# Performance work log

Measured on AMD Instinct MI355X. Metric: run time of the kernel, lower is better.

The kernel has to match this reference:

```python
import jax, jax.numpy as jnp
import numpy as np

B, N, C = 8, 4096, 768
H, M = 12, 64          # num_heads, num_landmarks
D = C // H             # head_dim = 64


def setup_inputs() -> dict:
    key = jax.random.key(0)
    k1, k2, k3, k4 = jax.random.split(key, 4)
    s = 0.02
    return {
        "x": jax.random.normal(k1, (B, N, C), dtype=jnp.float32),
        "w_qkv": jax.random.normal(k2, (3 * C, C), dtype=jnp.float32) * s,
        "w_proj": jax.random.normal(k3, (C, C), dtype=jnp.float32) * s,
        "b_proj": jax.random.normal(k4, (C,), dtype=jnp.float32) * s,
    }


def iterative_inv(mat, n_iter=6):
    # mat: [B, H, M, M]; Newton-Schulz cubic iteration for pseudo-inverse
    I = jnp.eye(mat.shape[-1], dtype=mat.dtype)
    K = mat
    # init: K^T / max_j(sum_i K_ij)  per (B,H)
    scale = jnp.max(jnp.sum(K, axis=-2), axis=-1)[:, :, None, None]
    V = jnp.swapaxes(K, -1, -2) / scale
    for _ in range(n_iter):
        KV = K @ V
        V = 0.25 * V @ (13.0 * I - KV @ (15.0 * I - KV @ (7.0 * I - KV)))
    return V


def reference(x, w_qkv, w_proj, b_proj):
    b, n, c = x.shape
    qkv = (x @ w_qkv.T).reshape(b, n, 3, H, D).transpose(2, 0, 3, 1, 4)  # [3,B,H,N,D]
    Q, K, V = qkv[0], qkv[1], qkv[2]
    Q = Q / (D ** 0.5)
    # landmark pooling (N % M == 0 path): segment means of length N//M
    Kl = K.reshape(b, H, M, n // M, D).mean(axis=-2)  # [B,H,M,D]
    Ql = Q.reshape(b, H, M, n // M, D).mean(axis=-2)  # [B,H,M,D]
    kernel1 = jax.nn.softmax(jnp.einsum('bhnd,bhmd->bhnm', Q, Kl), axis=-1)   # [B,H,N,M]
    kernel2 = jax.nn.softmax(jnp.einsum('bhmd,bhld->bhml', Ql, Kl), axis=-1)  # [B,H,M,M]
    kernel3 = jax.nn.softmax(jnp.einsum('bhmd,bhnd->bhmn', Ql, K), axis=-1)   # [B,H,M,N]
    SV = (kernel1 @ iterative_inv(kernel2)) @ (kernel3 @ V)  # [B,H,N,D]
    SV = SV.transpose(0, 2, 1, 3).reshape(b, n, c)
    out = SV @ w_proj.T + b_proj
    out = out + V.transpose(0, 2, 1, 3).reshape(b, n, c)
    return out
```

## Files before the change

kernel.cpp:

```cpp
#include <hip/hip_runtime.h>
#include <hip/hip_bf16.h>
#include <stdint.h>

typedef __bf16 bf16;
typedef __bf16 bf16x8 __attribute__((ext_vector_type(8)));
typedef __bf16 bf16x4 __attribute__((ext_vector_type(4)));
typedef float f32x4 __attribute__((ext_vector_type(4)));

#define B_ 8
#define N_ 4096
#define C_ 768
#define H_ 12
#define M_ 64
#define D_ 64
#define NT_ 32768
#define C3_ 2304

typedef __attribute__((address_space(3))) void lds_void_t;
typedef const __attribute__((address_space(1))) void gvoid_t;

__device__ __forceinline__ void gl_lds16(const void* gsrc, void* ldst) {
  __builtin_amdgcn_global_load_lds((gvoid_t*)(uintptr_t)gsrc,
                                   (lds_void_t*)(uintptr_t)ldst, 16, 0, 0);
}

__device__ __forceinline__ f32x4 mfma16(bf16x8 a, bf16x8 b, f32x4 c) {
  return __builtin_amdgcn_mfma_f32_16x16x32_bf16(a, b, c, 0, 0, 0);
}

#define VMW8 asm volatile("s_waitcnt vmcnt(8)" ::: "memory")
#define VMW4 asm volatile("s_waitcnt vmcnt(4)" ::: "memory")
#define VMW0 asm volatile("s_waitcnt vmcnt(0)" ::: "memory")
#define RAWBAR() { __builtin_amdgcn_sched_barrier(0); __builtin_amdgcn_s_barrier(); __builtin_amdgcn_sched_barrier(0); }

#define NX4   6291456
#define NW14  442368
#define NW24  147456
__global__ void k_cvt3(const float* __restrict__ x, bf16* __restrict__ xo,
                       const float* __restrict__ w1, bf16* __restrict__ w1o,
                       const float* __restrict__ w2, bf16* __restrict__ w2o) {
  const int stride = gridDim.x * blockDim.x;
  for (int i = blockIdx.x * blockDim.x + threadIdx.x; i < NX4 + NW14 + NW24; i += stride) {
    const float* src; bf16* dst; int idx;
    if (i < NX4)              { src = x;  dst = xo;  idx = i; }
    else if (i < NX4 + NW14)  { src = w1; dst = w1o; idx = i - NX4; }
    else                      { src = w2; dst = w2o; idx = i - NX4 - NW14; }
    f32x4 v = *(const f32x4*)(src + (size_t)idx * 4);
    bf16x4 o;
    o[0] = (bf16)v[0]; o[1] = (bf16)v[1]; o[2] = (bf16)v[2]; o[3] = (bf16)v[3];
    *(bf16x4*)(dst + (size_t)idx * 4) = o;
  }
}

__global__ __launch_bounds__(512, 2) void k_qkv(
    const bf16* __restrict__ xbf, const bf16* __restrict__ wbf,
    bf16* __restrict__ Qb, bf16* __restrict__ Kb, bf16* __restrict__ Vb,
    float* __restrict__ Qlf, float* __restrict__ Klf)
{
  __shared__ bf16 As[4][8192];
  __shared__ bf16 Bs[4][8192];
  const int t = threadIdx.x;
  const int wave = t >> 6, lane = t & 63;
  const int l15 = lane & 15, l16 = lane >> 4;

  const int bid = blockIdx.x;
  const int swz = (bid & 7) * 144 + (bid >> 3);
  const int bt = swz / 9, ct = swz % 9;
  const int row0 = bt * 256, ct0 = ct * 256;
  const int wr = wave >> 2, wc = wave & 3;

  const int srow = t >> 2;
  const int scol = (((t & 3) ^ ((t >> 3) & 3)) << 3);
  const bf16* gaBase = xbf + (size_t)(row0 + srow) * C_ + scol;
  const bf16* gbBase = wbf + (size_t)(ct0 + srow) * C_ + scol;

  const int aoff = (wr * 128 + l15) * 32 + ((l16 ^ ((l15 >> 1) & 3)) << 3);
  const int boff = (wc * 64 + l15) * 32 + ((l16 ^ ((l15 >> 1) & 3)) << 3);

  f32x4 acc[8][4] = {};
  bf16x8 afr0[4], afr1[4], bfr[2][4];

#define QSTAGE(kt3) {                                                            \
    const int sb_ = (kt3) & 3;                                                   \
    gl_lds16(gaBase + (kt3) * 32, &As[sb_][t * 8]);                              \
    gl_lds16(gbBase + (kt3) * 32, &Bs[sb_][t * 8]);                              \
    gl_lds16(gaBase + (size_t)128 * C_ + (kt3) * 32, &As[sb_][(t + 512) * 8]);   \
    gl_lds16(gbBase + (size_t)128 * C_ + (kt3) * 32, &Bs[sb_][(t + 512) * 8]); }

#define QKSTEP(kt, DO_STAGE, DO_NXT, VMW_, DO_BAR) {                             \
    if (DO_STAGE) QSTAGE((kt) + 3);                                             \
    { const bf16* asC = As[(kt) & 3];                                            \
      _Pragma("unroll")                                                          \
      for (int i = 0; i < 4; ++i)                                                \
        afr1[i] = *(const bf16x8*)&asC[aoff + (4 + i) * 512]; }                  \
    __builtin_amdgcn_s_setprio(1);                                               \
    _Pragma("unroll")                                                            \
    for (int i = 0; i < 4; ++i)                                                  \
      _Pragma("unroll")                                                          \
      for (int j = 0; j < 4; ++j)                                                \
        acc[i][j] = mfma16(afr0[i], bfr[(kt) & 1][j], acc[i][j]);                \
    __builtin_amdgcn_s_setprio(0);                                               \
    if (DO_NXT) {                                                                \
      const bf16* asN = As[((kt) + 1) & 3];                                      \
      const bf16* bsN = Bs[((kt) + 1) & 3];                                      \
      _Pragma("unroll")                                                          \
      for (int i = 0; i < 4; ++i)                                                \
        afr0[i] = *(const bf16x8*)&asN[aoff + i * 512];                          \
      _Pragma("unroll")                                                          \
      for (int j = 0; j < 4; ++j)                                                \
        bfr[((kt) + 1) & 1][j] = *(const bf16x8*)&bsN[boff + j * 512]; }         \
    __builtin_amdgcn_s_setprio(1);                                               \
    _Pragma("unroll")                                                            \
    for (int i = 0; i < 4; ++i)                                                  \
      _Pragma("unroll")                                                          \
      for (int j = 0; j < 4; ++j)                                                \
        acc[4 + i][j] = mfma16(afr1[i], bfr[(kt) & 1][j], acc[4 + i][j]);        \
    __builtin_amdgcn_s_setprio(0);                                               \
    VMW_;                                                                        \
    if (DO_BAR) RAWBAR(); }

  QSTAGE(0); QSTAGE(1); QSTAGE(2);
  VMW4;
  RAWBAR();
#pragma unroll
  for (int i = 0; i < 4; ++i) afr0[i] = *(const bf16x8*)&As[0][aoff + i * 512];
#pragma unroll
  for (int j = 0; j < 4; ++j) bfr[0][j] = *(const bf16x8*)&Bs[0][boff + j * 512];

  QKSTEP(0, 1, 1, VMW4, 1)  QKSTEP(1, 1, 1, VMW4, 1)  QKSTEP(2, 1, 1, VMW4, 1)
  QKSTEP(3, 1, 1, VMW4, 1)  QKSTEP(4, 1, 1, VMW4, 1)  QKSTEP(5, 1, 1, VMW4, 1)
  QKSTEP(6, 1, 1, VMW4, 1)  QKSTEP(7, 1, 1, VMW4, 1)  QKSTEP(8, 1, 1, VMW4, 1)
  QKSTEP(9, 1, 1, VMW4, 1)  QKSTEP(10, 1, 1, VMW4, 1) QKSTEP(11, 1, 1, VMW4, 1)
  QKSTEP(12, 1, 1, VMW4, 1) QKSTEP(13, 1, 1, VMW4, 1) QKSTEP(14, 1, 1, VMW4, 1)
  QKSTEP(15, 1, 1, VMW4, 1) QKSTEP(16, 1, 1, VMW4, 1) QKSTEP(17, 1, 1, VMW4, 1)
  QKSTEP(18, 1, 1, VMW4, 1) QKSTEP(19, 1, 1, VMW4, 1) QKSTEP(20, 1, 1, VMW4, 1)
  QKSTEP(21, 0, 1, VMW0, 1)
  QKSTEP(22, 0, 1, (void)0, 1)
  QKSTEP(23, 0, 0, (void)0, 0)

#undef QKSTEP
#undef QSTAGE

  const int colblock = ct0 + wc * 64;
  const int which = colblock / C_;
  const int h = (colblock % C_) / D_;
  const int b = row0 >> 12;
  const int n_base = (row0 & (N_ - 1)) + wr * 128;
  bf16* dst = (which == 0) ? Qb : (which == 1) ? Kb : Vb;
  const float scale = (which == 0) ? 0.125f : 1.0f;
  const size_t base = ((size_t)(b * H_ + h) * N_ + n_base) * D_;
#pragma unroll
  for (int i = 0; i < 8; ++i)
#pragma unroll
    for (int q = 0; q < 4; ++q) {
      const int rloc = i * 16 + l16 * 4 + q;
#pragma unroll
      for (int j = 0; j < 4; ++j) {
        const int d = j * 16 + l15;
        dst[base + (size_t)rloc * D_ + d] = (bf16)(acc[i][j][q] * scale);
      }
    }
  if (which < 2) {
    float* lmout = (which == 0) ? Qlf : Klf;
#pragma unroll
    for (int g = 0; g < 2; ++g) {
      const int m = (n_base >> 6) + g;
#pragma unroll
      for (int j = 0; j < 4; ++j) {
        float s = 0.f;
#pragma unroll
        for (int i = 4 * g; i < 4 * g + 4; ++i)
#pragma unroll
          for (int q = 0; q < 4; ++q) s += acc[i][j][q];
        s *= scale;
        s += __shfl_xor(s, 16);
        s += __shfl_xor(s, 32);
        if (l16 == 0)
          lmout[((size_t)(b * H_ + h) * M_ + m) * D_ + j * 16 + lane] = s * (1.0f / 64.0f);
      }
    }
  }
}

__global__ __launch_bounds__(512, 1) void k_inv(
    const float* __restrict__ Qlf, const float* __restrict__ Klf,
    float* __restrict__ pinv, bf16* __restrict__ Qlb, bf16* __restrict__ Klb)
{
  __shared__ float K2[4096];
  __shared__ float Vm[4096];
  __shared__ float KV[4096];
  __shared__ float T1[4096];
  __shared__ float U1[4096];
  __shared__ float tmp64[64];
  __shared__ float sscale;
  const int t = threadIdx.x;
  const int bh = blockIdx.x;
  const size_t off = (size_t)bh * 4096;
  for (int idx = t; idx < 4096; idx += 512) {
    const float q = Qlf[off + idx];
    T1[idx] = q;
    Qlb[off + idx] = (bf16)q;
  }
  for (int idx = t; idx < 4096; idx += 512) {
    const int r = idx >> 6, c = idx & 63;
    const float k = Klf[off + idx];
    U1[c * 64 + r] = k;
    Klb[off + idx] = (bf16)k;
  }
  __syncthreads();
  const int j0 = (t & 15) * 4;
  const int i0 = (t >> 4) * 2;

  auto MMstep = [&](const float* A, const float* Bm, float* O, float dg, float sg, float al) {
    float r2[2][4] = {};
    for (int k = 0; k < 64; ++k) {
      f32x4 bv = *(const f32x4*)&Bm[k * 64 + j0];
      const float a0 = A[(i0 + 0) * 64 + k];
      const float a1 = A[(i0 + 1) * 64 + k];
#pragma unroll
      for (int jj = 0; jj < 4; ++jj) { r2[0][jj] += a0 * bv[jj]; r2[1][jj] += a1 * bv[jj]; }
    }
#pragma unroll
    for (int ii = 0; ii < 2; ++ii)
#pragma unroll
      for (int jj = 0; jj < 4; ++jj)
        O[(i0 + ii) * 64 + j0 + jj] = al * (dg * A[(i0 + ii) * 64 + (j0 + jj)] + sg * r2[ii][jj]);
    __syncthreads();
  };

  {
    float r2[2][4] = {};
    for (int k = 0; k < 64; ++k) {
      f32x4 bv = *(const f32x4*)&U1[k * 64 + j0];
      const float a0 = T1[(i0 + 0) * 64 + k];
      const float a1 = T1[(i0 + 1) * 64 + k];
#pragma unroll
      for (int jj = 0; jj < 4; ++jj) { r2[0][jj] += a0 * bv[jj]; r2[1][jj] += a1 * bv[jj]; }
    }
#pragma unroll
    for (int ii = 0; ii < 2; ++ii)
#pragma unroll
      for (int jj = 0; jj < 4; ++jj)
        K2[(i0 + ii) * 64 + j0 + jj] = __expf(r2[ii][jj]);
  }
  __syncthreads();
  if (t < 64) {
    float s = 0.f;
    for (int k = 0; k < 64; ++k) s += K2[t * 64 + k];
    tmp64[t] = 1.0f / s;
  }
  __syncthreads();
  for (int idx = t; idx < 4096; idx += 512) K2[idx] *= tmp64[idx >> 6];
  __syncthreads();
  if (t < 64) {
    float s = 0.f;
    for (int i = 0; i < 64; ++i) s += K2[i * 64 + t];
    tmp64[t] = s;
  }
  __syncthreads();
  if (t == 0) {
    float mx = tmp64[0];
    for (int j2 = 1; j2 < 64; ++j2) mx = fmaxf(mx, tmp64[j2]);
    sscale = 1.0f / mx;
  }
  __syncthreads();
  for (int idx = t; idx < 4096; idx += 512) {
    const int r = idx >> 6, c = idx & 63;
    Vm[idx] = K2[c * 64 + r] * sscale;
  }
  __syncthreads();

  float* pV = Vm;
  float* pT = T1;
  for (int it = 0; it < 6; ++it) {
    MMstep(K2, pV, KV, 0.f, 1.f, 1.f);
    MMstep(KV, KV, pT, 7.f, -1.f, 1.f);
    MMstep(KV, pT, U1, 15.f, -1.f, 1.f);
    MMstep(pV, U1, pT, 13.f, -1.f, 0.25f);
    float* sw = pV; pV = pT; pT = sw;
  }
  for (int idx = t; idx < 4096; idx += 512) pinv[off + idx] = pV[idx];
}

__global__ __launch_bounds__(256, 2) void k_k3v(
    const bf16* __restrict__ Qlb, const bf16* __restrict__ Kb, const bf16* __restrict__ Vb,
    float* __restrict__ Zpart, float* __restrict__ rspart)
{
  __shared__ bf16 Qls[64 * 64];
  __shared__ bf16 Ks[128 * 64];
  __shared__ bf16 Vs[128 * 64];
  __shared__ bf16 Ps[64 * 128];
  __shared__ float rs[64];
  const int t = threadIdx.x, wave = t >> 6, lane = t & 63;
  const int l15 = lane & 15, l16 = lane >> 4;
  const int key = l15 & 7;
  const int bh = blockIdx.x >> 3;
  const int chunk = blockIdx.x & 7;
  const size_t kvbase = (size_t)bh * N_ * D_ + (size_t)chunk * 512 * D_;
  const int srow8 = t >> 3;
  const int ssw = (((t & 7) ^ ((t >> 3) & 7)) << 3);
  {
    const bf16* g = Qlb + (size_t)bh * 4096;
    gl_lds16(g + (size_t)srow8 * 64 + ssw, &Qls[t * 8]);
    gl_lds16(g + (size_t)(32 + srow8) * 64 + ssw, &Qls[(t + 256) * 8]);
  }
  if (t < 64) rs[t] = 0.f;
  f32x4 z[4] = {};
  for (int st = 0; st < 4; ++st) {
    const bf16* gk = Kb + kvbase + (size_t)st * 128 * D_;
    const bf16* gv = Vb + kvbase + (size_t)st * 128 * D_;
#pragma unroll
    for (int c = 0; c < 4; ++c) {
      gl_lds16(gk + (size_t)(c * 32 + srow8) * 64 + ssw, &Ks[(t + c * 256) * 8]);
      gl_lds16(gv + (t + c * 256) * 8, &Vs[(t + c * 256) * 8]);
    }
    __syncthreads();
    f32x4 sacc[4][2] = {};
#pragma unroll
    for (int kk = 0; kk < 2; ++kk) {
      bf16x8 af[4], bk[2];
#pragma unroll
      for (int i = 0; i < 4; ++i)
        af[i] = *(const bf16x8*)&Qls[(i * 16 + l15) * 64 + (((kk * 4 + l16) ^ key) << 3)];
#pragma unroll
      for (int j2 = 0; j2 < 2; ++j2)
        bk[j2] = *(const bf16x8*)&Ks[(wave * 32 + j2 * 16 + l15) * 64 + (((kk * 4 + l16) ^ key) << 3)];
#pragma unroll
      for (int i = 0; i < 4; ++i)
#pragma unroll
        for (int j2 = 0; j2 < 2; ++j2)
          sacc[i][j2] = mfma16(af[i], bk[j2], sacc[i][j2]);
    }
#pragma unroll
    for (int i = 0; i < 4; ++i)
#pragma unroll
      for (int q = 0; q < 4; ++q) {
        const float e0 = __expf(sacc[i][0][q]);
        const float e1 = __expf(sacc[i][1][q]);
        const int m = i * 16 + l16 * 4 + q;
        const int mk = m & 7;
        Ps[m * 128 + ((((wave * 4 + (l15 >> 3)) ^ mk) << 3) | (l15 & 7))] = (bf16)e0;
        Ps[m * 128 + ((((wave * 4 + 2 + (l15 >> 3)) ^ mk) << 3) | (l15 & 7))] = (bf16)e1;
        float p = e0 + e1;
        p += __shfl_xor(p, 1); p += __shfl_xor(p, 2);
        p += __shfl_xor(p, 4); p += __shfl_xor(p, 8);
        if (l15 == 0) atomicAdd(&rs[m], p);
      }
    __syncthreads();
#pragma unroll
    for (int kk = 0; kk < 4; ++kk) {
      const int kbase = kk * 32 + 8 * l16;
      const int d = wave * 16 + l15;
      bf16x8 bv;
#pragma unroll
      for (int e = 0; e < 8; ++e) bv[e] = Vs[(kbase + e) * 64 + d];
#pragma unroll
      for (int i = 0; i < 4; ++i) {
        bf16x8 ap = *(const bf16x8*)&Ps[(i * 16 + l15) * 128 + (((kk * 4 + l16) ^ key) << 3)];
        z[i] = mfma16(ap, bv, z[i]);
      }
    }
    __syncthreads();
  }
  const size_t zbase = ((size_t)bh * 8 + chunk) * 4096;
#pragma unroll
  for (int i = 0; i < 4; ++i)
#pragma unroll
    for (int q = 0; q < 4; ++q) {
      const int m = i * 16 + l16 * 4 + q;
      const int d = wave * 16 + l15;
      Zpart[zbase + m * 64 + d] = z[i][q];
    }
  if (t < 64) rspart[((size_t)bh * 8 + chunk) * 64 + t] = rs[t];
}

__global__ __launch_bounds__(256, 1) void k_comb(
    const float* __restrict__ pinv, const float* __restrict__ Zpart,
    const float* __restrict__ rspart, bf16* __restrict__ Wtb)
{
  __shared__ float Pv[4096];
  __shared__ float Zn[4096];
  __shared__ float rsum[64];
  const int t = threadIdx.x, bh = blockIdx.x;
  const size_t off = (size_t)bh * 4096;
  const float* zp = Zpart + (size_t)bh * 8 * 4096;
  const float* rp = rspart + (size_t)bh * 8 * 64;
  for (int idx = t; idx < 4096; idx += 256) Pv[idx] = pinv[off + idx];
  if (t < 64) {
    float s = 0.f;
#pragma unroll
    for (int c = 0; c < 8; ++c) s += rp[c * 64 + t];
    rsum[t] = s;
  }
  __syncthreads();
  for (int idx = t; idx < 4096; idx += 256) {
    float s = 0.f;
#pragma unroll
    for (int c = 0; c < 8; ++c) s += zp[c * 4096 + idx];
    Zn[idx] = s / rsum[idx >> 6];
  }
  __syncthreads();
  const int j0 = (t & 15) * 4, i0 = (t >> 4) * 4;
  float r[4][4] = {{0.f}};
  for (int k = 0; k < 64; ++k) {
    f32x4 bv = *(const f32x4*)&Zn[k * 64 + j0];
    float a[4];
#pragma unroll
    for (int ii = 0; ii < 4; ++ii) a[ii] = Pv[(i0 + ii) * 64 + k];
#pragma unroll
    for (int ii = 0; ii < 4; ++ii)
#pragma unroll
      for (int jj = 0; jj < 4; ++jj) r[ii][jj] += a[ii] * bv[jj];
  }
#pragma unroll
  for (int ii = 0; ii < 4; ++ii)
#pragma unroll
    for (int jj = 0; jj < 4; ++jj)
      Wtb[off + (size_t)(j0 + jj) * 64 + (i0 + ii)] = (bf16)r[ii][jj];
}

__global__ __launch_bounds__(256, 3) void k_sv(
    const bf16* __restrict__ Qb, const bf16* __restrict__ Klb,
    const bf16* __restrict__ Wtb, bf16* __restrict__ SVb)
{
  __shared__ bf16 Qs[128 * 64];
  __shared__ bf16 Kls[64 * 64];
  __shared__ bf16 Wts[64 * 64];
  __shared__ bf16 Ps[128 * 64];
  const int t = threadIdx.x, wave = t >> 6, lane = t & 63;
  const int l15 = lane & 15, l16 = lane >> 4;
  const int key = l15 & 7;
  const int bh = blockIdx.x >> 5;
  const int nt = blockIdx.x & 31;
  const int b = bh / H_, h = bh % H_;
  const int srow8 = t >> 3;
  const int ssw = (((t & 7) ^ ((t >> 3) & 7)) << 3);
  {
    const bf16* gq = Qb + (size_t)bh * N_ * D_ + (size_t)nt * 128 * D_;
#pragma unroll
    for (int c = 0; c < 4; ++c)
      gl_lds16(gq + (size_t)(c * 32 + srow8) * 64 + ssw, &Qs[(t + c * 256) * 8]);
    const bf16* gkl = Klb + (size_t)bh * 4096;
    gl_lds16(gkl + (size_t)srow8 * 64 + ssw, &Kls[t * 8]);
    gl_lds16(gkl + (size_t)(32 + srow8) * 64 + ssw, &Kls[(t + 256) * 8]);
    const bf16* gw = Wtb + (size_t)bh * 4096;
    gl_lds16(gw + (size_t)srow8 * 64 + ssw, &Wts[t * 8]);
    gl_lds16(gw + (size_t)(32 + srow8) * 64 + ssw, &Wts[(t + 256) * 8]);
  }
  __syncthreads();
  f32x4 sacc[2][4] = {};
#pragma unroll
  for (int kk = 0; kk < 2; ++kk) {
    bf16x8 af[2], bl[4];
#pragma unroll
    for (int r = 0; r < 2; ++r)
      af[r] = *(const bf16x8*)&Qs[(wave * 32 + r * 16 + l15) * 64 + (((kk * 4 + l16) ^ key) << 3)];
#pragma unroll
    for (int j = 0; j < 4; ++j)
      bl[j] = *(const bf16x8*)&Kls[(j * 16 + l15) * 64 + (((kk * 4 + l16) ^ key) << 3)];
#pragma unroll
    for (int r = 0; r < 2; ++r)
#pragma unroll
      for (int j = 0; j < 4; ++j)
        sacc[r][j] = mfma16(af[r], bl[j], sacc[r][j]);
  }
#pragma unroll
  for (int r = 0; r < 2; ++r)
#pragma unroll
    for (int q = 0; q < 4; ++q) {
      float e[4]; float s = 0.f;
#pragma unroll
      for (int j = 0; j < 4; ++j) { e[j] = __expf(sacc[r][j][q]); s += e[j]; }
      s += __shfl_xor(s, 1); s += __shfl_xor(s, 2);
      s += __shfl_xor(s, 4); s += __shfl_xor(s, 8);
      const float is = 1.0f / s;
      const int row = wave * 32 + r * 16 + l16 * 4 + q;
      const int rk = row & 7;
#pragma unroll
      for (int j = 0; j < 4; ++j) {
        const int col = j * 16 + l15;
        Ps[row * 64 + ((((col >> 3) ^ rk) << 3) | (col & 7))] = (bf16)(e[j] * is);
      }
    }
  __syncthreads();
  f32x4 oacc[2][4] = {};
#pragma unroll
  for (int kk = 0; kk < 2; ++kk) {
    bf16x8 af[2], bw[4];
#pragma unroll
    for (int r = 0; r < 2; ++r)
      af[r] = *(const bf16x8*)&Ps[(wave * 32 + r * 16 + l15) * 64 + (((kk * 4 + l16) ^ key) << 3)];
#pragma unroll
    for (int j = 0; j < 4; ++j)
      bw[j] = *(const bf16x8*)&Wts[(j * 16 + l15) * 64 + (((kk * 4 + l16) ^ key) << 3)];
#pragma unroll
    for (int r = 0; r < 2; ++r)
#pragma unroll
      for (int j = 0; j < 4; ++j)
        oacc[r][j] = mfma16(af[r], bw[j], oacc[r][j]);
  }
  const size_t outbase = ((size_t)b * N_ + (size_t)nt * 128) * C_ + h * 64;
#pragma unroll
  for (int r = 0; r < 2; ++r)
#pragma unroll
    for (int q = 0; q < 4; ++q) {
      const int row = wave * 32 + r * 16 + l16 * 4 + q;
#pragma unroll
      for (int j = 0; j < 4; ++j)
        SVb[outbase + (size_t)row * C_ + j * 16 + l15] = (bf16)(oacc[r][j][q]);
    }
}

__global__ __launch_bounds__(256, 3) void k_proj(
    const bf16* __restrict__ SVb, const bf16* __restrict__ wpb,
    const float* __restrict__ bproj, const bf16* __restrict__ Vb,
    float* __restrict__ outp)
{
  __shared__ bf16 As[4][4096];
  __shared__ bf16 Bs[4][4096];
  const int t = threadIdx.x;
  const int wave = t >> 6, lane = t & 63;
  const int l15 = lane & 15, l16 = lane >> 4;
  const int bid = blockIdx.x;
  const int swz = (bid & 7) * 192 + (bid >> 3);
  const int bt = swz / 6, ct = swz % 6;
  const int row0 = bt * 128, col0 = ct * 128;
  const int wr = wave >> 1, wc = wave & 1;

  const int srow = t >> 2;
  const int scol = (((t & 3) ^ ((t >> 3) & 3)) << 3);
  const bf16* ga = SVb + (size_t)(row0 + srow) * C_ + scol;
  const bf16* gb = wpb + (size_t)(col0 + srow) * C_ + scol;

  const int aoff = (wr * 64 + l15) * 32 + ((l16 ^ ((l15 >> 1) & 3)) << 3);
  const int boff = (wc * 64 + l15) * 32 + ((l16 ^ ((l15 >> 1) & 3)) << 3);

  f32x4 acc[4][4] = {};
  bf16x8 afr[2][4], bfr[2][4];

#define PSTAGE(kt3) {                                                          \
    const int sb_ = (kt3) & 3;                                                 \
    gl_lds16(ga + (kt3) * 32, &As[sb_][t * 8]);                                \
    gl_lds16(gb + (kt3) * 32, &Bs[sb_][t * 8]);                                \
    gl_lds16(ga + (size_t)64 * C_ + (kt3) * 32, &As[sb_][(t + 256) * 8]);      \
    gl_lds16(gb + (size_t)64 * C_ + (kt3) * 32, &Bs[sb_][(t + 256) * 8]); }

#define PKSTEP(kt, DO_STAGE, DO_NXT, VMW_, DO_BAR) {                           \
    if (DO_STAGE) PSTAGE((kt) + 3);                                            \
    if (DO_NXT) {                                                              \
      const bf16* asN = As[((kt) + 1) & 3];                                    \
      const bf16* bsN = Bs[((kt) + 1) & 3];                                    \
      _Pragma("unroll")                                                        \
      for (int i = 0; i < 4; ++i)                                              \
        afr[((kt) + 1) & 1][i] = *(const bf16x8*)&asN[aoff + i * 512];         \
      _Pragma("unroll")                                                        \
      for (int j = 0; j < 4; ++j)                                              \
        bfr[((kt) + 1) & 1][j] = *(const bf16x8*)&bsN[boff + j * 512]; }       \
    __builtin_amdgcn_s_setprio(1);                                             \
    _Pragma("unroll")                                                          \
    for (int i = 0; i < 4; ++i)                                                \
      _Pragma("unroll")                                                        \
      for (int j = 0; j < 4; ++j)                                              \
        acc[i][j] = mfma16(afr[(kt) & 1][i], bfr[(kt) & 1][j], acc[i][j]);     \
    __builtin_amdgcn_s_setprio(0);                                             \
    VMW_;                                                                      \
    if (DO_BAR) RAWBAR(); }

  PSTAGE(0); PSTAGE(1); PSTAGE(2);
  VMW4;
  RAWBAR();
#pragma unroll
  for (int i = 0; i < 4; ++i) afr[0][i] = *(const bf16x8*)&As[0][aoff + i * 512];
#pragma unroll
  for (int j = 0; j < 4; ++j) bfr[0][j] = *(const bf16x8*)&Bs[0][boff + j * 512];

  PKSTEP(0, 1, 1, VMW4, 1)  PKSTEP(1, 1, 1, VMW4, 1)  PKSTEP(2, 1, 1, VMW4, 1)
  PKSTEP(3, 1, 1, VMW4, 1)  PKSTEP(4, 1, 1, VMW4, 1)  PKSTEP(5, 1, 1, VMW4, 1)
  PKSTEP(6, 1, 1, VMW4, 1)  PKSTEP(7, 1, 1, VMW4, 1)  PKSTEP(8, 1, 1, VMW4, 1)
  PKSTEP(9, 1, 1, VMW4, 1)  PKSTEP(10, 1, 1, VMW4, 1) PKSTEP(11, 1, 1, VMW4, 1)
  PKSTEP(12, 1, 1, VMW4, 1) PKSTEP(13, 1, 1, VMW4, 1) PKSTEP(14, 1, 1, VMW4, 1)
  PKSTEP(15, 1, 1, VMW4, 1) PKSTEP(16, 1, 1, VMW4, 1) PKSTEP(17, 1, 1, VMW4, 1)
  PKSTEP(18, 1, 1, VMW4, 1) PKSTEP(19, 1, 1, VMW4, 1) PKSTEP(20, 1, 1, VMW4, 1)
  PKSTEP(21, 0, 1, VMW0, 1)
  PKSTEP(22, 0, 1, (void)0, 1)
  PKSTEP(23, 0, 0, (void)0, 0)

#undef PKSTEP
#undef PSTAGE

#pragma unroll
  for (int i = 0; i < 4; ++i)
#pragma unroll
    for (int q = 0; q < 4; ++q) {
      const int row = row0 + wr * 64 + i * 16 + l16 * 4 + q;
      const int b = row >> 12, n = row & (N_ - 1);
#pragma unroll
      for (int j = 0; j < 4; ++j) {
        const int col = col0 + wc * 64 + j * 16 + l15;
        const int h = col >> 6, d = col & 63;
        const float v = acc[i][j][q] + bproj[col] +
                        (float)Vb[((size_t)(b * H_ + h) * N_ + n) * D_ + d];
        outp[(size_t)row * C_ + col] = v;
      }
    }
}

extern "C" void kernel_launch(void* const* d_in, const int* in_sizes, int n_in,
                              void* d_out, int out_size, void* d_ws, size_t ws_size,
                              hipStream_t stream) {
  const float* x = (const float*)d_in[0];
  const float* wqkv = (const float*)d_in[1];
  const float* wproj = (const float*)d_in[2];
  const float* bproj = (const float*)d_in[3];
  float* outp = (float*)d_out;
  char* ws = (char*)d_ws;

  size_t off = 0;
  auto take = [&](size_t bytes) { char* p = ws + off; off += bytes; return p; };
  bf16* xbf     = (bf16*)take(50331648);
  bf16* wqkvbf  = (bf16*)take(3538944);
  bf16* wprojbf = (bf16*)take(1179648);
  bf16* Qb      = (bf16*)take(50331648);
  bf16* Kb      = (bf16*)take(50331648);
  bf16* Vb      = (bf16*)take(50331648);
  float* Qlf    = (float*)take(1572864);
  float* Klf    = (float*)take(1572864);
  bf16* Qlb     = (bf16*)take(786432);
  bf16* Klb     = (bf16*)take(786432);
  float* pinvp  = (float*)take(1572864);
  float* Zpart  = (float*)take(12582912);
  float* rspart = (float*)take(196608);
  bf16* Wtb     = (bf16*)take(786432);
  bf16* SVb     = xbf;

  k_cvt3<<<2048, 256, 0, stream>>>(x, xbf, wqkv, wqkvbf, wproj, wprojbf);
  k_qkv<<<1152, 512, 0, stream>>>(xbf, wqkvbf, Qb, Kb, Vb, Qlf, Klf);
  k_inv<<<96, 512, 0, stream>>>(Qlf, Klf, pinvp, Qlb, Klb);
  k_k3v<<<768, 256, 0, stream>>>(Qlb, Kb, Vb, Zpart, rspart);
  k_comb<<<96, 256, 0, stream>>>(pinvp, Zpart, rspart, Wtb);
  k_sv<<<96 * 32, 256, 0, stream>>>(Qb, Klb, Wtb, SVb);
  k_proj<<<1536, 256, 0, stream>>>(SVb, wprojbf, bproj, Vb, outp);
}
```

Baseline: 362.6 us.

## Double-buffer K/V tiles in k_k3v with smaller stages and higher occupancy

Rewrites the k_k3v inner loop to process 64-key stages from a two-slot LDS ring, prefetching the next stage's K and V with async global-to-LDS loads while the current stage computes. The aim is to overlap global load latency with the QK and PV MFMA work instead of stalling on a barrier after every load. Halving the stage size keeps LDS usage roughly constant, which allows launch bounds to rise to three blocks per CU. The cost is twice as many stages and barriers and fewer MFMAs per stage, which may cut per-stage efficiency.

```diff
diff --git a/kernel.cpp b/kernel.cpp
--- a/kernel.cpp
+++ b/kernel.cpp
@@ -282,14 +282,14 @@
   for (int idx = t; idx < 4096; idx += 512) pinv[off + idx] = pV[idx];
 }
 
-__global__ __launch_bounds__(256, 2) void k_k3v(
+__global__ __launch_bounds__(256, 3) void k_k3v(
     const bf16* __restrict__ Qlb, const bf16* __restrict__ Kb, const bf16* __restrict__ Vb,
     float* __restrict__ Zpart, float* __restrict__ rspart)
 {
   __shared__ bf16 Qls[64 * 64];
-  __shared__ bf16 Ks[128 * 64];
-  __shared__ bf16 Vs[128 * 64];
-  __shared__ bf16 Ps[64 * 128];
+  __shared__ bf16 Ks[2][64 * 64];
+  __shared__ bf16 Vs[2][64 * 64];
+  __shared__ bf16 Ps[64 * 64];
   __shared__ float rs[64];
   const int t = threadIdx.x, wave = t >> 6, lane = t & 63;
   const int l15 = lane & 15, l16 = lane >> 4;
@@ -299,69 +299,73 @@
   const size_t kvbase = (size_t)bh * N_ * D_ + (size_t)chunk * 512 * D_;
   const int srow8 = t >> 3;
   const int ssw = (((t & 7) ^ ((t >> 3) & 7)) << 3);
+
+#define KVSTAGE(st, buf) {                                                      \
+    const bf16* gk = Kb + kvbase + (size_t)(st) * 64 * D_;                      \
+    const bf16* gv = Vb + kvbase + (size_t)(st) * 64 * D_;                      \
+    gl_lds16(gk + (size_t)srow8 * 64 + ssw, &Ks[buf][t * 8]);                   \
+    gl_lds16(gk + (size_t)(32 + srow8) * 64 + ssw, &Ks[buf][(t + 256) * 8]);    \
+    gl_lds16(gv + t * 8, &Vs[buf][t * 8]);                                      \
+    gl_lds16(gv + (t + 256) * 8, &Vs[buf][(t + 256) * 8]); }
+
   {
     const bf16* g = Qlb + (size_t)bh * 4096;
     gl_lds16(g + (size_t)srow8 * 64 + ssw, &Qls[t * 8]);
     gl_lds16(g + (size_t)(32 + srow8) * 64 + ssw, &Qls[(t + 256) * 8]);
   }
   if (t < 64) rs[t] = 0.f;
+  KVSTAGE(0, 0);
+  VMW0;
+  RAWBAR();
+
   f32x4 z[4] = {};
-  for (int st = 0; st < 4; ++st) {
-    const bf16* gk = Kb + kvbase + (size_t)st * 128 * D_;
-    const bf16* gv = Vb + kvbase + (size_t)st * 128 * D_;
-#pragma unroll
-    for (int c = 0; c < 4; ++c) {
-      gl_lds16(gk + (size_t)(c * 32 + srow8) * 64 + ssw, &Ks[(t + c * 256) * 8]);
-      gl_lds16(gv + (t + c * 256) * 8, &Vs[(t + c * 256) * 8]);
-    }
-    __syncthreads();
-    f32x4 sacc[4][2] = {};
+  for (int st = 0; st < 8; ++st) {
+    const int buf = st & 1;
+    if (st < 7) KVSTAGE(st + 1, buf ^ 1);
+    f32x4 sacc[4] = {};
 #pragma unroll
     for (int kk = 0; kk < 2; ++kk) {
-      bf16x8 af[4], bk[2];
+      bf16x8 af[4], bk;
 #pragma unroll
       for (int i = 0; i < 4; ++i)
         af[i] = *(const bf16x8*)&Qls[(i * 16 + l15) * 64 + (((kk * 4 + l16) ^ key) << 3)];
-#pragma unroll
-      for (int j2 = 0; j2 < 2; ++j2)
-        bk[j2] = *(const bf16x8*)&Ks[(wave * 32 + j2 * 16 + l15) * 64 + (((kk * 4 + l16) ^ key) << 3)];
+      bk = *(const bf16x8*)&Ks[buf][(wave * 16 + l15) * 64 + (((kk * 4 + l16) ^ key) << 3)];
 #pragma unroll
       for (int i = 0; i < 4; ++i)
-#pragma unroll
-        for (int j2 = 0; j2 < 2; ++j2)
-          sacc[i][j2] = mfma16(af[i], bk[j2], sacc[i][j2]);
+        sacc[i] = mfma16(af[i], bk, sacc[i]);
     }
 #pragma unroll
     for (int i = 0; i < 4; ++i)
 #pragma unroll
       for (int q = 0; q < 4; ++q) {
-        const float e0 = __expf(sacc[i][0][q]);
-        const float e1 = __expf(sacc[i][1][q]);
+        const float e0 = __expf(sacc[i][q]);
         const int m = i * 16 + l16 * 4 + q;
         const int mk = m & 7;
-        Ps[m * 128 + ((((wave * 4 + (l15 >> 3)) ^ mk) << 3) | (l15 & 7))] = (bf16)e0;
-        Ps[m * 128 + ((((wave * 4 + 2 + (l15 >> 3)) ^ mk) << 3) | (l15 & 7))] = (bf16)e1;
-        float p = e0 + e1;
+        Ps[m * 64 + ((((wave * 2 + (l15 >> 3)) ^ mk) << 3) | (l15 & 7))] = (bf16)e0;
+        float p = e0;
         p += __shfl_xor(p, 1); p += __shfl_xor(p, 2);
         p += __shfl_xor(p, 4); p += __shfl_xor(p, 8);
         if (l15 == 0) atomicAdd(&rs[m], p);
       }
-    __syncthreads();
-#pragma unroll
-    for (int kk = 0; kk < 4; ++kk) {
+    RAWBAR();
+#pragma unroll
+    for (int kk = 0; kk < 2; ++kk) {
       const int kbase = kk * 32 + 8 * l16;
       const int d = wave * 16 + l15;
       bf16x8 bv;
 #pragma unroll
-      for (int e = 0; e < 8; ++e) bv[e] = Vs[(kbase + e) * 64 + d];
+      for (int e = 0; e < 8; ++e) bv[e] = Vs[buf][(kbase + e) * 64 + d];
 #pragma unroll
       for (int i = 0; i < 4; ++i) {
-        bf16x8 ap = *(const bf16x8*)&Ps[(i * 16 + l15) * 128 + (((kk * 4 + l16) ^ key) << 3)];
+        bf16x8 ap = *(const bf16x8*)&Ps[(i * 16 + l15) * 64 + (((kk * 4 + l16) ^ key) << 3)];
         z[i] = mfma16(ap, bv, z[i]);
       }
     }
-    __syncthreads();
-  }
+    if (st < 7) VMW0;
+    RAWBAR();
+  }
+#undef KVSTAGE
+
   const size_t zbase = ((size_t)bh * 8 + chunk) * 4096;
 #pragma unroll
   for (int i = 0; i < 4; ++i)
```

Result: no change. 365.2 us (+0.7%).
